# Kernel tuning notes

Measured on AMD Instinct MI355X. Metric: run time of the kernel, lower is better.

Reference implementation:

```python
import jax, jax.numpy as jnp
import numpy as np

B, N, D = 8, 2048, 512
DK, DV = 512, 512


def setup_inputs() -> dict:
    key = jax.random.key(0)
    ks = jax.random.split(key, 7)
    s = 1.0 / np.sqrt(D)
    return {
        "x": jax.random.normal(ks[0], (B, N, D), dtype=jnp.float32),
        "Wq": jax.random.normal(ks[1], (D, DK), dtype=jnp.float32) * s,
        "bq": jnp.zeros((DK,), dtype=jnp.float32),
        "Wk": jax.random.normal(ks[2], (D, DK), dtype=jnp.float32) * s,
        "bk": jnp.zeros((DK,), dtype=jnp.float32),
        "Wv": jax.random.normal(ks[3], (D, DV), dtype=jnp.float32) * s,
        "bv": jnp.zeros((DV,), dtype=jnp.float32),
    }


def reference(x, Wq, bq, Wk, bk, Wv, bv):
    # norm = 1/sqrt(dim_k); original divides softmax output by norm (post-softmax scale)
    inv_norm = jnp.sqrt(jnp.asarray(DK, dtype=x.dtype))  # 1/norm = sqrt(dim_k)
    Q = x @ Wq + bq  # [B,N,DK]
    K = x @ Wk + bk  # [B,N,DK]
    V = x @ Wv + bv  # [B,N,DV]
    scores = jnp.einsum("bnd,bmd->bnm", Q, K)  # [B,N,N] (NO pre-softmax scaling)
    att = jax.nn.softmax(scores, axis=-1) * inv_norm  # faithful post-softmax scale
    return jnp.einsum("bnm,bmv->bnv", att, V)  # [B,N,DV]
```

## Files before the change

kernel.cpp:

```cpp
#include <hip/hip_runtime.h>
#include <stdint.h>
#include <stddef.h>


typedef _Float16 f16_t;
typedef _Float16 f16x8 __attribute__((ext_vector_type(8)));
typedef float    f32x4 __attribute__((ext_vector_type(4)));

__device__ __forceinline__ f32x4 mfma_h(f16x8 a, f16x8 b, f32x4 c) {
  return __builtin_amdgcn_mfma_f32_16x16x32_f16(a, b, c, 0, 0, 0);
}

__device__ __forceinline__ void gl_lds16(const void* g, void* lds) {
  __builtin_amdgcn_global_load_lds(
      (const __attribute__((address_space(1))) unsigned int*)g,
      (__attribute__((address_space(3))) unsigned int*)lds, 16, 0, 0);
}

__device__ __forceinline__ void stage_tile(f16_t* lds, const f16_t* g,
                                           size_t gstride, int wave, int lane) {
  const int l8 = lane >> 3;
  const int lslot = (lane & 7) ^ l8;
  #pragma unroll
  for (int c = 0; c < 4; ++c) {
    const int chunk = wave * 4 + c;
    const int row = chunk * 8 + l8;
    gl_lds16(g + (size_t)row * gstride + lslot * 8, lds + chunk * 512);
  }
}

__device__ __forceinline__ f16x8 lds_frag(const f16_t* buf, int R, int slot) {
  return *(const f16x8*)&buf[R * 64 + (((slot ^ (R & 7)) & 7) << 3)];
}

__device__ __forceinline__ unsigned int fenc(float f) {
  unsigned int u = __float_as_uint(f);
  return (u & 0x80000000u) ? ~u : (u | 0x80000000u);
}
__device__ __forceinline__ float fdec(unsigned int e) {
  unsigned int u = (e & 0x80000000u) ? (e & 0x7fffffffu) : ~e;
  return __uint_as_float(u);
}

__device__ __forceinline__ int xcd_swz(int id, int nwg) {
  return (id & 7) * (nwg >> 3) + (id >> 3);
}

__global__ __launch_bounds__(256) void k_conv_x(const float* __restrict__ x,
                                                f16_t* __restrict__ x16) {
  const int i = (blockIdx.x * 256 + threadIdx.x) * 8;
  const float4 a = *(const float4*)&x[i];
  const float4 b = *(const float4*)&x[i + 4];
  float v[8] = {a.x, a.y, a.z, a.w, b.x, b.y, b.z, b.w};
  f16x8 h;
  #pragma unroll
  for (int j = 0; j < 8; ++j) h[j] = (f16_t)v[j];
  *(f16x8*)&x16[i] = h;
}

__global__ __launch_bounds__(256) void k_conv_w(const float* __restrict__ Wq,
                                                const float* __restrict__ Wk,
                                                const float* __restrict__ Wv,
                                                f16_t* __restrict__ Wt) {
  __shared__ float t[64][65];
  const int p = blockIdx.z;
  const float* __restrict__ W = (p == 0) ? Wq : (p == 1) ? Wk : Wv;
  const int n0 = blockIdx.x * 64, k0 = blockIdx.y * 64;
  const int tx = threadIdx.x & 63, ty = threadIdx.x >> 6;
  #pragma unroll
  for (int j = 0; j < 16; ++j)
    t[ty * 16 + j][tx] = W[(size_t)(k0 + ty * 16 + j) * 512 + n0 + tx];
  __syncthreads();
  #pragma unroll
  for (int j = 0; j < 16; ++j) {
    const int nl = ty * 16 + j;
    Wt[(size_t)p * 262144 + (size_t)(n0 + nl) * 512 + k0 + tx] =
        (f16_t)t[tx][nl];
  }
}

__global__ __launch_bounds__(256, 2) void k_proj(
    const f16_t* __restrict__ x16, const f16_t* __restrict__ Wt,
    const float* __restrict__ bq, const float* __restrict__ bk,
    const float* __restrict__ bv,
    f16_t* __restrict__ Q, f16_t* __restrict__ K, f16_t* __restrict__ Vt)
{
  __shared__ __align__(16) unsigned char smem[34816];
  f16_t* A = (f16_t*)smem;
  f16_t* B = (f16_t*)(smem + 16384);

  const int wg = xcd_swz(blockIdx.x, 1536);
  const int mt = wg / 12, jt = wg % 12;
  const int which = jt >> 2;
  const int jb = (jt & 3) * 128;

  const int tid = threadIdx.x, lane = tid & 63, wave = tid >> 6;
  const int wr = wave >> 1, wc = wave & 1, l15 = lane & 15, lg = lane >> 4;
  const int rowbase = mt * 128;

  const f16_t* Wbase = Wt + (size_t)which * 262144 + (size_t)jb * 512;

  f32x4 acc[4][4] = {};

  for (int kb = 0; kb < 512; kb += 64) {
    __syncthreads();
    stage_tile(A, x16 + (size_t)rowbase * 512 + kb, 512, wave, lane);
    stage_tile(B, Wbase + kb, 512, wave, lane);
    __syncthreads();
    #pragma unroll
    for (int h = 0; h < 2; ++h) {
      const int slot0 = h * 4 + lg;
      f16x8 af[4], bf[4];
      #pragma unroll
      for (int g = 0; g < 4; ++g) {
        af[g] = lds_frag(A, wr * 64 + g * 16 + l15, slot0);
        bf[g] = lds_frag(B, wc * 64 + g * 16 + l15, slot0);
      }
      #pragma unroll
      for (int i = 0; i < 4; ++i)
        #pragma unroll
        for (int j = 0; j < 4; ++j)
          acc[i][j] = mfma_h(af[i], bf[j], acc[i][j]);
    }
  }

  if (which != 2) {
    f16_t* __restrict__ O = (which == 0) ? Q : K;
    const float* __restrict__ bb = (which == 0) ? bq : bk;
    #pragma unroll
    for (int j = 0; j < 4; ++j) {
      const int jl = jb + wc * 64 + j * 16 + l15;
      const float bias = bb[jl];
      #pragma unroll
      for (int i = 0; i < 4; ++i)
        #pragma unroll
        for (int r = 0; r < 4; ++r) {
          const int row = rowbase + wr * 64 + i * 16 + lg * 4 + r;
          O[(size_t)row * 512 + jl] = (f16_t)(acc[i][j][r] + bias);
        }
    }
  } else {
    __syncthreads();
    f16_t* vtl = (f16_t*)smem;
    #pragma unroll
    for (int j = 0; j < 4; ++j) {
      const int jj = wc * 64 + j * 16 + l15;
      const float bias = bv[jb + jj];
      #pragma unroll
      for (int i = 0; i < 4; ++i)
        #pragma unroll
        for (int r = 0; r < 4; ++r) {
          const int ii = wr * 64 + i * 16 + lg * 4 + r;
          vtl[jj * 136 + ii] = (f16_t)(acc[i][j][r] + bias);
        }
    }
    __syncthreads();
    const int dv = tid >> 1, hf = tid & 1;
    const int bat = rowbase >> 11, n0 = rowbase & 2047;
    f16_t* __restrict__ dst =
        &Vt[((size_t)bat * 512 + jb + dv) * 2048 + n0 + hf * 64];
    const f16_t* src = &vtl[dv * 136 + hf * 64];
    #pragma unroll
    for (int s = 0; s < 8; ++s)
      *(f16x8*)&dst[s * 8] = *(const f16x8*)&src[s * 8];
  }
}

__global__ __launch_bounds__(256, 2) void k_qk(const f16_t* __restrict__ Q,
                                               const f16_t* __restrict__ K,
                                               float* __restrict__ S,
                                               unsigned int* __restrict__ mEnc)
{
  __shared__ __align__(16) f16_t A[128 * 64];
  __shared__ __align__(16) f16_t Bt[128 * 64];

  const int wg = xcd_swz(blockIdx.x, 2048);
  const int bat = wg >> 8, mt = (wg >> 4) & 15, nt = wg & 15;
  const int tid = threadIdx.x, lane = tid & 63, wave = tid >> 6;
  const int wr = wave >> 1, wc = wave & 1, l15 = lane & 15, lg = lane >> 4;

  f32x4 acc[4][4] = {};
  const f16_t* Abase = Q + ((size_t)bat * 2048 + mt * 128) * 512;
  const f16_t* Bbase = K + ((size_t)bat * 2048 + nt * 128) * 512;

  for (int kb = 0; kb < 512; kb += 64) {
    __syncthreads();
    stage_tile(A, Abase + kb, 512, wave, lane);
    stage_tile(Bt, Bbase + kb, 512, wave, lane);
    __syncthreads();
    #pragma unroll
    for (int h = 0; h < 2; ++h) {
      const int slot0 = h * 4 + lg;
      f16x8 af[4], bf[4];
      #pragma unroll
      for (int g = 0; g < 4; ++g) {
        af[g] = lds_frag(A, wr * 64 + g * 16 + l15, slot0);
        bf[g] = lds_frag(Bt, wc * 64 + g * 16 + l15, slot0);
      }
      #pragma unroll
      for (int i = 0; i < 4; ++i)
        #pragma unroll
        for (int j = 0; j < 4; ++j)
          acc[i][j] = mfma_h(af[i], bf[j], acc[i][j]);
    }
  }

  #pragma unroll
  for (int i = 0; i < 4; ++i)
    #pragma unroll
    for (int r = 0; r < 4; ++r) {
      const int ii = mt * 128 + wr * 64 + i * 16 + lg * 4 + r;
      float mv = fmaxf(fmaxf(acc[i][0][r], acc[i][1][r]),
                       fmaxf(acc[i][2][r], acc[i][3][r]));
      mv = fmaxf(mv, __shfl_xor(mv, 1));
      mv = fmaxf(mv, __shfl_xor(mv, 2));
      mv = fmaxf(mv, __shfl_xor(mv, 4));
      mv = fmaxf(mv, __shfl_xor(mv, 8));
      if (l15 == 0)
        atomicMax(&mEnc[(size_t)bat * 2048 + ii], fenc(mv));
      #pragma unroll
      for (int j = 0; j < 4; ++j) {
        const int jj = nt * 128 + wc * 64 + j * 16 + l15;
        S[((size_t)bat * 2048 + ii) * 2048 + jj] = acc[i][j][r];
      }
    }
}

__global__ __launch_bounds__(256, 2) void k_pv3(const float* __restrict__ S,
                                                const f16_t* __restrict__ Vt,
                                                const unsigned int* __restrict__ mEnc,
                                                float* __restrict__ out)
{
  __shared__ __align__(16) f16_t P[64 * 64];
  __shared__ __align__(16) f16_t Vl[256 * 64];
  __shared__ float lred[64][4];

  const int id = blockIdx.x;
  const int bat = id & 7, qt = (id >> 3) & 31, dvh = id >> 8;
  const int tid = threadIdx.x, lane = tid & 63, wave = tid >> 6;
  const int l15 = lane & 15, lg = lane >> 4;

  const int qs = tid >> 2;
  const int cq = tid & 3;
  const float LOG2E = 1.4426950408889634f;
  const float mls = fdec(mEnc[bat * 2048 + qt * 64 + qs]) * LOG2E;
  const float* __restrict__ srow =
      S + ((size_t)bat * 2048 + qt * 64 + qs) * 2048;
  const f16_t* Vbase = Vt + ((size_t)bat * 512 + dvh * 256) * 2048;

  f32x4 acc[4][4] = {};
  float l_part = 0.f;

  float4 s0 = *(const float4*)&srow[cq * 16];
  float4 s1 = *(const float4*)&srow[cq * 16 + 4];
  float4 s2 = *(const float4*)&srow[cq * 16 + 8];
  float4 s3 = *(const float4*)&srow[cq * 16 + 12];

  for (int kb = 0; kb < 2048; kb += 64) {
    asm volatile("s_waitcnt lgkmcnt(0)\n\ts_barrier" ::: "memory");
    __builtin_amdgcn_sched_barrier(0);
    stage_tile(Vl, Vbase + kb, 2048, wave, lane);
    stage_tile(Vl + 128 * 64, Vbase + (size_t)128 * 2048 + kb, 2048, wave, lane);
    __builtin_amdgcn_sched_barrier(0);
    float e[16] = {s0.x, s0.y, s0.z, s0.w, s1.x, s1.y, s1.z, s1.w,
                   s2.x, s2.y, s2.z, s2.w, s3.x, s3.y, s3.z, s3.w};
    const int kn = (kb + 64) & 2047;
    s0 = *(const float4*)&srow[kn + cq * 16];
    s1 = *(const float4*)&srow[kn + cq * 16 + 4];
    s2 = *(const float4*)&srow[kn + cq * 16 + 8];
    s3 = *(const float4*)&srow[kn + cq * 16 + 12];
    __builtin_amdgcn_sched_barrier(0);
    #pragma unroll
    for (int g2 = 0; g2 < 2; ++g2) {
      f16x8 p;
      #pragma unroll
      for (int j = 0; j < 8; ++j) {
        const float ev =
            __builtin_amdgcn_exp2f(fmaf(e[g2 * 8 + j], LOG2E, -mls));
        l_part += ev;
        p[j] = (f16_t)ev;
      }
      const int slot = cq * 2 + g2;
      *(f16x8*)&P[qs * 64 + ((slot ^ (qs & 7)) << 3)] = p;
    }
    asm volatile("s_waitcnt vmcnt(4) lgkmcnt(0)\n\ts_barrier" ::: "memory");
    __builtin_amdgcn_sched_barrier(0);
    #pragma unroll
    for (int ks = 0; ks < 2; ++ks) {
      const int slot0 = ks * 4 + lg;
      f16x8 af[4], bf[4];
      #pragma unroll
      for (int g = 0; g < 4; ++g) {
        af[g] = lds_frag(P, g * 16 + l15, slot0);
        bf[g] = lds_frag(Vl, wave * 64 + g * 16 + l15, slot0);
      }
      #pragma unroll
      for (int i = 0; i < 4; ++i)
        #pragma unroll
        for (int j = 0; j < 4; ++j)
          acc[i][j] = mfma_h(af[i], bf[j], acc[i][j]);
    }
  }

  __syncthreads();
  lred[qs][cq] = l_part;
  __syncthreads();

  #pragma unroll
  for (int i = 0; i < 4; ++i)
    #pragma unroll
    for (int r = 0; r < 4; ++r) {
      const int ql = i * 16 + lg * 4 + r;
      const float l = lred[ql][0] + lred[ql][1] + lred[ql][2] + lred[ql][3];
      const float sc = 22.62741699796952f / l;
      const size_t orow = ((size_t)bat * 2048 + qt * 64 + ql) * 512;
      #pragma unroll
      for (int j = 0; j < 4; ++j) {
        const int dv = dvh * 256 + wave * 64 + j * 16 + l15;
        out[orow + dv] = acc[i][j][r] * sc;
      }
    }
}

extern "C" void kernel_launch(void* const* d_in, const int* in_sizes, int n_in,
                              void* d_out, int out_size, void* d_ws, size_t ws_size,
                              hipStream_t stream) {
  const float* x  = (const float*)d_in[0];
  const float* Wq = (const float*)d_in[1];
  const float* bq = (const float*)d_in[2];
  const float* Wk = (const float*)d_in[3];
  const float* bk = (const float*)d_in[4];
  const float* Wv = (const float*)d_in[5];
  const float* bv = (const float*)d_in[6];
  float* out = (float*)d_out;

  char* ws = (char*)d_ws;
  f16_t* x16 = (f16_t*)(ws + 0);
  f16_t* Q   = (f16_t*)(ws + 16777216);
  f16_t* K   = (f16_t*)(ws + 33554432);
  f16_t* Vt  = (f16_t*)(ws + 50331648);
  float* S   = (float*)(ws + 67108864);
  f16_t* Wt  = (f16_t*)(ws + 201326592);
  unsigned int* mEnc = (unsigned int*)(ws + 202899456);

  (void)hipMemsetAsync(mEnc, 0, 65536, stream);
  k_conv_x<<<4096, 256, 0, stream>>>(x, x16);
  k_conv_w<<<dim3(8, 8, 3), 256, 0, stream>>>(Wq, Wk, Wv, Wt);
  k_proj<<<1536, 256, 0, stream>>>(x16, Wt, bq, bk, bv, Q, K, Vt);
  k_qk<<<2048, 256, 0, stream>>>(Q, K, S, mEnc);
  k_pv3<<<512, 256, 0, stream>>>(S, Vt, mEnc, out);
}
```

Before: 161.2 us.

## Load V fragments directly to registers and double-buffer P in PV kernel

The PV kernel no longer stages V tiles into shared memory. Each wave now loads its MFMA B-operand fragments straight from global memory into registers, and the P (softmax probability) tile is double-buffered so the next tile's exponentials are computed while the current tile is multiplied. This removes the LDS staging traffic for V and one barrier wait per iteration. In exchange it relies on uncoalesced-ish per-lane global loads with latency that is less hidden and adds register pressure.

Result: slower. 188.1 us (+16.7%).

```diff
diff --git a/kernel.cpp b/kernel.cpp
--- a/kernel.cpp
+++ b/kernel.cpp
@@ -226,13 +226,12 @@
     }
 }
 
-__global__ __launch_bounds__(256, 2) void k_pv3(const float* __restrict__ S,
+__global__ __launch_bounds__(256, 2) void k_pv4(const float* __restrict__ S,
                                                 const f16_t* __restrict__ Vt,
                                                 const unsigned int* __restrict__ mEnc,
                                                 float* __restrict__ out)
 {
-  __shared__ __align__(16) f16_t P[64 * 64];
-  __shared__ __align__(16) f16_t Vl[256 * 64];
+  __shared__ __align__(16) f16_t P[2][64 * 64];
   __shared__ float lred[64][4];
 
   const int id = blockIdx.x;
@@ -245,31 +244,28 @@
   const float LOG2E = 1.4426950408889634f;
   const float mls = fdec(mEnc[bat * 2048 + qt * 64 + qs]) * LOG2E;
   const float* __restrict__ srow =
-      S + ((size_t)bat * 2048 + qt * 64 + qs) * 2048;
-  const f16_t* Vbase = Vt + ((size_t)bat * 512 + dvh * 256) * 2048;
+      S + ((size_t)bat * 2048 + qt * 64 + qs) * 2048 + cq * 16;
+
+  const size_t vdv = (size_t)bat * 512 + dvh * 256 + wave * 64 + l15;
+  const f16_t* __restrict__ vb0 = Vt + (vdv +  0) * 2048;
+  const f16_t* __restrict__ vb1 = Vt + (vdv + 16) * 2048;
+  const f16_t* __restrict__ vb2 = Vt + (vdv + 32) * 2048;
+  const f16_t* __restrict__ vb3 = Vt + (vdv + 48) * 2048;
 
   f32x4 acc[4][4] = {};
   float l_part = 0.f;
 
-  float4 s0 = *(const float4*)&srow[cq * 16];
-  float4 s1 = *(const float4*)&srow[cq * 16 + 4];
-  float4 s2 = *(const float4*)&srow[cq * 16 + 8];
-  float4 s3 = *(const float4*)&srow[cq * 16 + 12];
-
-  for (int kb = 0; kb < 2048; kb += 64) {
-    asm volatile("s_waitcnt lgkmcnt(0)\n\ts_barrier" ::: "memory");
-    __builtin_amdgcn_sched_barrier(0);
-    stage_tile(Vl, Vbase + kb, 2048, wave, lane);
-    stage_tile(Vl + 128 * 64, Vbase + (size_t)128 * 2048 + kb, 2048, wave, lane);
-    __builtin_amdgcn_sched_barrier(0);
-    float e[16] = {s0.x, s0.y, s0.z, s0.w, s1.x, s1.y, s1.z, s1.w,
-                   s2.x, s2.y, s2.z, s2.w, s3.x, s3.y, s3.z, s3.w};
-    const int kn = (kb + 64) & 2047;
-    s0 = *(const float4*)&srow[kn + cq * 16];
-    s1 = *(const float4*)&srow[kn + cq * 16 + 4];
-    s2 = *(const float4*)&srow[kn + cq * 16 + 8];
-    s3 = *(const float4*)&srow[kn + cq * 16 + 12];
-    __builtin_amdgcn_sched_barrier(0);
+  float4 p0 = *(const float4*)&srow[0];
+  float4 p1 = *(const float4*)&srow[4];
+  float4 p2 = *(const float4*)&srow[8];
+  float4 p3 = *(const float4*)&srow[12];
+  float4 s0 = *(const float4*)&srow[64];
+  float4 s1 = *(const float4*)&srow[64 + 4];
+  float4 s2 = *(const float4*)&srow[64 + 8];
+  float4 s3 = *(const float4*)&srow[64 + 12];
+  {
+    float e[16] = {p0.x, p0.y, p0.z, p0.w, p1.x, p1.y, p1.z, p1.w,
+                   p2.x, p2.y, p2.z, p2.w, p3.x, p3.y, p3.z, p3.w};
     #pragma unroll
     for (int g2 = 0; g2 < 2; ++g2) {
       f16x8 p;
@@ -281,24 +277,67 @@
         p[j] = (f16_t)ev;
       }
       const int slot = cq * 2 + g2;
-      *(f16x8*)&P[qs * 64 + ((slot ^ (qs & 7)) << 3)] = p;
-    }
-    asm volatile("s_waitcnt vmcnt(4) lgkmcnt(0)\n\ts_barrier" ::: "memory");
+      *(f16x8*)&P[0][qs * 64 + ((slot ^ (qs & 7)) << 3)] = p;
+    }
+  }
+
+  for (int t = 0; t < 32; ++t) {
+    const int kb = t * 64;
+    asm volatile("s_waitcnt lgkmcnt(0)\n\ts_barrier" ::: "memory");
     __builtin_amdgcn_sched_barrier(0);
+
+    f16x8 v00, v01, v10, v11, v20, v21, v30, v31;
+    {
+      const int c0 = kb + lg * 8, c1 = kb + (4 + lg) * 8;
+      v00 = *(const f16x8*)&vb0[c0];  v01 = *(const f16x8*)&vb0[c1];
+      v10 = *(const f16x8*)&vb1[c0];  v11 = *(const f16x8*)&vb1[c1];
+      v20 = *(const f16x8*)&vb2[c0];  v21 = *(const f16x8*)&vb2[c1];
+      v30 = *(const f16x8*)&vb3[c0];  v31 = *(const f16x8*)&vb3[c1];
+    }
+
+    if (t < 31) {
+      float e[16] = {s0.x, s0.y, s0.z, s0.w, s1.x, s1.y, s1.z, s1.w,
+                     s2.x, s2.y, s2.z, s2.w, s3.x, s3.y, s3.z, s3.w};
+      const int kn = ((t + 2) * 64) & 2047;
+      s0 = *(const float4*)&srow[kn];
+      s1 = *(const float4*)&srow[kn + 4];
+      s2 = *(const float4*)&srow[kn + 8];
+      s3 = *(const float4*)&srow[kn + 12];
+      f16_t* Pn = P[(t + 1) & 1];
+      #pragma unroll
+      for (int g2 = 0; g2 < 2; ++g2) {
+        f16x8 p;
+        #pragma unroll
+        for (int j = 0; j < 8; ++j) {
+          const float ev =
+              __builtin_amdgcn_exp2f(fmaf(e[g2 * 8 + j], LOG2E, -mls));
+          l_part += ev;
+          p[j] = (f16_t)ev;
+        }
+        const int slot = cq * 2 + g2;
+        *(f16x8*)&Pn[qs * 64 + ((slot ^ (qs & 7)) << 3)] = p;
+      }
+    }
+
+    const f16_t* Pc = P[t & 1];
     #pragma unroll
     for (int ks = 0; ks < 2; ++ks) {
       const int slot0 = ks * 4 + lg;
-      f16x8 af[4], bf[4];
-      #pragma unroll
-      for (int g = 0; g < 4; ++g) {
-        af[g] = lds_frag(P, g * 16 + l15, slot0);
-        bf[g] = lds_frag(Vl, wave * 64 + g * 16 + l15, slot0);
-      }
-      #pragma unroll
-      for (int i = 0; i < 4; ++i)
-        #pragma unroll
-        for (int j = 0; j < 4; ++j)
-          acc[i][j] = mfma_h(af[i], bf[j], acc[i][j]);
+      f16x8 af[4];
+      #pragma unroll
+      for (int g = 0; g < 4; ++g)
+        af[g] = lds_frag(Pc, g * 16 + l15, slot0);
+      const f16x8 b0 = ks ? v01 : v00;
+      const f16x8 b1 = ks ? v11 : v10;
+      const f16x8 b2 = ks ? v21 : v20;
+      const f16x8 b3 = ks ? v31 : v30;
+      #pragma unroll
+      for (int i = 0; i < 4; ++i) {
+        acc[i][0] = mfma_h(af[i], b0, acc[i][0]);
+        acc[i][1] = mfma_h(af[i], b1, acc[i][1]);
+        acc[i][2] = mfma_h(af[i], b2, acc[i][2]);
+        acc[i][3] = mfma_h(af[i], b3, acc[i][3]);
+      }
     }
   }
 
@@ -348,5 +387,5 @@
   k_conv_w<<<dim3(8, 8, 3), 256, 0, stream>>>(Wq, Wk, Wv, Wt);
   k_proj<<<1536, 256, 0, stream>>>(x16, Wt, bq, bk, bv, Q, K, Vt);
   k_qk<<<2048, 256, 0, stream>>>(Q, K, S, mEnc);
-  k_pv3<<<512, 256, 0, stream>>>(S, Vt, mEnc, out);
-}
+  k_pv4<<<512, 256, 0, stream>>>(S, Vt, mEnc, out);
+}
```
